# Performance work log

Measured on AMD Instinct MI355X. Metric: run time of the kernel, lower is better.

## Reference

```python
import jax, jax.numpy as jnp
import numpy as np

N = 100000
E = 1600000
IN_C, HID_C, OUT_C = 512, 128, 64
BN_EPS = 1e-5


def _add_self_loops(edge_index, n):
    loops = jnp.arange(n, dtype=edge_index.dtype)
    row = jnp.concatenate([edge_index[0], loops])
    col = jnp.concatenate([edge_index[1], loops])
    return row, col


def gcn_conv(x, W, b, row, col, n):
    # PyG GCNConv: linear first, then symmetric-normalized aggregation
    h = x @ W                                        # [N, out]
    ones = jnp.ones(row.shape[0], dtype=x.dtype)
    deg = jax.ops.segment_sum(ones, col, num_segments=n)   # in-degree incl. self-loop
    dinv = jax.lax.rsqrt(deg)                        # deg >= 1 due to self-loops
    norm = dinv[row] * dinv[col]                     # [E2]
    msg = h[row] * norm[:, None]                     # gather + scale
    out = jax.ops.segment_sum(msg, col, num_segments=n)    # scatter-add
    return out + b


def batchnorm_train(x, gamma, beta):
    mu = jnp.mean(x, axis=0)
    var = jnp.mean((x - mu) ** 2, axis=0)            # biased var, as torch BN
    return (x - mu) * jax.lax.rsqrt(var + BN_EPS) * gamma + beta


def setup_inputs() -> dict:
    key = jax.random.key(0)
    ks = jax.random.split(key, 8)
    x = jax.random.normal(ks[0], (N, IN_C), dtype=jnp.float32)
    edge_index = jax.random.randint(ks[1], (2, E), 0, N, dtype=jnp.int64)
    W1 = jax.random.normal(ks[2], (IN_C, HID_C), dtype=jnp.float32) / np.sqrt(IN_C)
    b1 = jnp.zeros((HID_C,), dtype=jnp.float32)
    gamma = jnp.ones((HID_C,), dtype=jnp.float32)
    beta = jnp.zeros((HID_C,), dtype=jnp.float32)
    W2 = jax.random.normal(ks[3], (HID_C, OUT_C), dtype=jnp.float32) / np.sqrt(HID_C)
    b2 = jnp.zeros((OUT_C,), dtype=jnp.float32)
    return {"x": x, "edge_index": edge_index, "W1": W1, "b1": b1,
            "gamma": gamma, "beta": beta, "W2": W2, "b2": b2}


def reference(x, edge_index, W1, b1, gamma, beta, W2, b2):
    row, col = _add_self_loops(edge_index, N)
    h = gcn_conv(x, W1, b1, row, col, N)
    h = batchnorm_train(h, gamma, beta)
    h = jax.nn.relu(h)
    # dropout: identity (deterministic reference)
    out = gcn_conv(h, W2, b2, row, col, N)
    return out
```

## Files before the change

### kernel.cpp

```cpp
#include <hip/hip_runtime.h>

#define NN 100000
#define NE 1600000
#define INC 512
#define HID 128
#define OUTC 64
#define BN_EPS 1e-5f

#define GS_B 1024
#define NSCB 98

#define NBLK 256
#define CHUNK (NE / NBLK)
#define BSH 8
#define NBUK ((NN + 255) >> 8)

typedef __attribute__((ext_vector_type(8))) short short8v;
typedef __attribute__((ext_vector_type(4))) float f32x4;

__device__ __forceinline__ unsigned short f2bf(float f) {
    unsigned u = __float_as_uint(f);
    u += 0x7FFFu + ((u >> 16) & 1u);
    return (unsigned short)(u >> 16);
}

__device__ __forceinline__ unsigned cvtpk(float lo, float hi) {
    unsigned r;
    asm("v_cvt_pk_bf16_f32 %0, %1, %2" : "=v"(r) : "v"(lo), "v"(hi));
    return r;
}

__device__ __forceinline__ float bflo(unsigned u) { return __uint_as_float(u << 16); }
__device__ __forceinline__ float bfhi(unsigned u) { return __uint_as_float(u & 0xFFFF0000u); }


__global__ __launch_bounds__(256) void k_bhist(const int* __restrict__ col, int* __restrict__ bhist,
                                               float* bnsum, float* bnsumsq) {
    __shared__ int lc[NBUK];
    int tid = threadIdx.x, blk = blockIdx.x;
    if (blk == 0 && tid < HID) { bnsum[tid] = 0.f; bnsumsq[tid] = 0.f; }
    for (int i = tid; i < NBUK; i += 256) lc[i] = 0;
    __syncthreads();
    int s = blk * CHUNK, e = s + CHUNK;
    for (int j = s + tid; j < e; j += 256)
        atomicAdd(&lc[col[j] >> BSH], 1);
    __syncthreads();
    for (int i = tid; i < NBUK; i += 256)
        bhist[i * NBLK + blk] = lc[i];
}

__global__ void k_gscanA(const int* __restrict__ src, int* __restrict__ dst,
                         int* __restrict__ bsum, int n) {
    __shared__ int s[GS_B];
    int tid = threadIdx.x;
    int i = blockIdx.x * GS_B + tid;
    int v = (i < n) ? src[i] : 0;
    s[tid] = v;
    __syncthreads();
    for (int off = 1; off < GS_B; off <<= 1) {
        int t = (tid >= off) ? s[tid - off] : 0;
        __syncthreads();
        s[tid] += t;
        __syncthreads();
    }
    if (i < n) dst[i] = s[tid] - v;
    if (tid == GS_B - 1) bsum[blockIdx.x] = s[tid];
}

__global__ void k_gscanB(int* bsum, int nb) {
    __shared__ int s[256];
    int tid = threadIdx.x;
    for (int i = tid; i < nb; i += blockDim.x) s[i] = bsum[i];
    __syncthreads();
    if (tid == 0) {
        int run = 0;
        for (int i = 0; i < nb; ++i) { int t = s[i]; s[i] = run; run += t; }
    }
    __syncthreads();
    for (int i = tid; i < nb; i += blockDim.x) bsum[i] = s[i];
}

__global__ __launch_bounds__(256) void k_bpart(const int* __restrict__ row, const int* __restrict__ col,
                                               const int* __restrict__ sb, const int* __restrict__ sbsum,
                                               unsigned* __restrict__ ebuk) {
    __shared__ int lcur[NBUK];
    int tid = threadIdx.x, blk = blockIdx.x;
    for (int i = tid; i < NBUK; i += 256) {
        int idx = i * NBLK + blk;
        lcur[i] = sb[idx] + sbsum[idx >> 10];
    }
    __syncthreads();
    int s = blk * CHUNK, e = s + CHUNK;
    for (int j = s + tid; j < e; j += 256) {
        int r = row[j], c = col[j];
        int p = atomicAdd(&lcur[c >> BSH], 1);
        ebuk[p] = (unsigned)r | ((unsigned)(c & 255) << 24);
    }
}

__global__ __launch_bounds__(256) void k_nprep(const unsigned* __restrict__ ebuk,
                                               const int* __restrict__ sb, const int* __restrict__ sbsum,
                                               int* __restrict__ deg, int* __restrict__ rowptr) {
    __shared__ int lc[256];
    __shared__ int sc[256];
    int b = blockIdx.x, tid = threadIdx.x;
    lc[tid] = 0;
    __syncthreads();
    int i0 = b * NBLK;
    int s = sb[i0] + sbsum[i0 >> 10];
    int e2 = (b + 1 < NBUK) ? (sb[i0 + NBLK] + sbsum[(i0 + NBLK) >> 10]) : NE;
    for (int j = s + tid; j < e2; j += 256)
        atomicAdd(&lc[ebuk[j] >> 24], 1);
    __syncthreads();
    int v = lc[tid];
    sc[tid] = v;
    __syncthreads();
    for (int off = 1; off < 256; off <<= 1) {
        int t = (tid >= off) ? sc[tid - off] : 0;
        __syncthreads();
        sc[tid] += t;
        __syncthreads();
    }
    int node = (b << BSH) + tid;
    if (node < NN) {
        deg[node] = v;
        rowptr[node] = s + sc[tid] - v;
    }
    if (b == NBUK - 1 && tid == 0) rowptr[NN] = NE;
}

__global__ __launch_bounds__(256) void k_bfill(const unsigned* __restrict__ ebuk,
                                               const int* __restrict__ sb, const int* __restrict__ sbsum,
                                               const int* __restrict__ rowptr, const int* __restrict__ deg,
                                               unsigned* __restrict__ csr) {
    __shared__ int lcur[256];
    int b = blockIdx.x, tid = threadIdx.x;
    int node0 = b << BSH;
    int node = node0 + tid;
    lcur[tid] = (node < NN) ? rowptr[node] : 0;
    __syncthreads();
    int i0 = b * NBLK;
    int s = sb[i0] + sbsum[i0 >> 10];
    int e2 = (b + 1 < NBUK) ? (sb[i0 + NBLK] + sbsum[(i0 + NBLK) >> 10]) : NE;
    for (int j = s + tid; j < e2; j += 256) {
        unsigned rc = ebuk[j];
        int li = rc >> 24;
        int r = rc & 0xFFFFFF;
        int p = atomicAdd(&lcur[li], 1);
        csr[p] = (unsigned)r | ((unsigned)deg[r] << 17);
    }
}


__global__ void k_prepW1(const float* __restrict__ W1, unsigned short* __restrict__ W1T) {
    int i = blockIdx.x * 256 + threadIdx.x;
    int k = i >> 7, n = i & 127;
    W1T[(size_t)n * INC + k] = f2bf(W1[i]);
}


#define G1BK 64
#define APAD 72

__global__ __launch_bounds__(256) void k_gemm1m(const float* __restrict__ x,
                                                const unsigned short* __restrict__ W1T,
                                                unsigned short* __restrict__ h1b) {
    __shared__ unsigned short As[64][APAD];
    __shared__ unsigned short Bs[128][APAD];
    int tid = threadIdx.x;
    int m0 = blockIdx.x * 64;
    int w = tid >> 6;
    int lane = tid & 63;

    f32x4 acc[4][2];
    #pragma unroll
    for (int mr = 0; mr < 4; ++mr)
        #pragma unroll
        for (int cb = 0; cb < 2; ++cb) acc[mr][cb] = (f32x4){0.f, 0.f, 0.f, 0.f};

    int ar = tid >> 2;
    int ak = (tid & 3) * 16;
    int arow = m0 + ar; if (arow >= NN) arow = NN - 1;
    const float* xr = x + (size_t)arow * INC;
    int br = tid >> 1;
    int bk = (tid & 1) * 32;
    const unsigned short* wr = W1T + (size_t)br * INC;

    int frow = lane & 15;
    int fk = (lane >> 4) * 8;

    float4 pv[4];
    short8v pb[4];
    #pragma unroll
    for (int q = 0; q < 4; ++q) pv[q] = *(const float4*)(xr + ak + q * 4);
    #pragma unroll
    for (int q = 0; q < 4; ++q) pb[q] = *(const short8v*)(wr + bk + q * 8);

    for (int k0 = 0; k0 < INC; k0 += G1BK) {
        #pragma unroll
        for (int q = 0; q < 4; ++q)
            *(uint2*)&As[ar][ak + q * 4] = make_uint2(cvtpk(pv[q].x, pv[q].y), cvtpk(pv[q].z, pv[q].w));
        #pragma unroll
        for (int q = 0; q < 4; ++q)
            *(short8v*)&Bs[br][bk + q * 8] = pb[q];
        __syncthreads();
        if (k0 + G1BK < INC) {
            #pragma unroll
            for (int q = 0; q < 4; ++q) pv[q] = *(const float4*)(xr + k0 + G1BK + ak + q * 4);
            #pragma unroll
            for (int q = 0; q < 4; ++q) pb[q] = *(const short8v*)(wr + k0 + G1BK + bk + q * 8);
        }
        #pragma unroll
        for (int kk = 0; kk < G1BK; kk += 32) {
            short8v a[4], b[2];
            #pragma unroll
            for (int mr = 0; mr < 4; ++mr)
                a[mr] = *(const short8v*)&As[16 * mr + frow][kk + fk];
            #pragma unroll
            for (int cb = 0; cb < 2; ++cb)
                b[cb] = *(const short8v*)&Bs[32 * w + 16 * cb + frow][kk + fk];
            #pragma unroll
            for (int mr = 0; mr < 4; ++mr)
                #pragma unroll
                for (int cb = 0; cb < 2; ++cb)
                    acc[mr][cb] = __builtin_amdgcn_mfma_f32_16x16x32_bf16(b[cb], a[mr], acc[mr][cb], 0, 0, 0);
        }
        __syncthreads();
    }
    int ncol = lane & 15;
    int r4 = (lane >> 4) * 4;
    #pragma unroll
    for (int mr = 0; mr < 4; ++mr) {
        int node = m0 + 16 * mr + ncol;
        if (node < NN) {
            #pragma unroll
            for (int cb = 0; cb < 2; ++cb) {
                int ch = 32 * w + 16 * cb + r4;
                *(uint2*)&h1b[(size_t)node * HID + ch] =
                    make_uint2(cvtpk(acc[mr][cb][0], acc[mr][cb][1]),
                               cvtpk(acc[mr][cb][2], acc[mr][cb][3]));
            }
        }
    }
}


__global__ __launch_bounds__(256) void k_agg1(const unsigned short* __restrict__ h1b,
                                              const int* __restrict__ deg,
                                              const int* __restrict__ rowptr, const unsigned* __restrict__ csr,
                                              const float* __restrict__ b1, unsigned* __restrict__ aggb) {
    int node = blockIdx.x * 4 + (threadIdx.x >> 6);
    int lane = threadIdx.x & 63;
    const unsigned* hp = (const unsigned*)h1b;
    size_t base = (size_t)node * 64 + lane;
    float dnf = (float)(deg[node] + 1);
    float di = rsqrtf(dnf);
    float wself = di * di;
    unsigned hv = hp[base];
    float sx = wself * bflo(hv);
    float sy = wself * bfhi(hv);
    int s = rowptr[node], e = rowptr[node + 1];
    int j = s;
    for (; j + 4 <= e; j += 4) {
        unsigned c0 = csr[j], c1 = csr[j + 1], c2 = csr[j + 2], c3 = csr[j + 3];
        int r0 = c0 & 0x1FFFF, r1 = c1 & 0x1FFFF, r2 = c2 & 0x1FFFF, r3 = c3 & 0x1FFFF;
        unsigned v0 = hp[(size_t)r0 * 64 + lane];
        unsigned v1 = hp[(size_t)r1 * 64 + lane];
        unsigned v2 = hp[(size_t)r2 * 64 + lane];
        unsigned v3 = hp[(size_t)r3 * 64 + lane];
        float w0 = rsqrtf(dnf * (float)((c0 >> 17) + 1));
        float w1 = rsqrtf(dnf * (float)((c1 >> 17) + 1));
        float w2 = rsqrtf(dnf * (float)((c2 >> 17) + 1));
        float w3 = rsqrtf(dnf * (float)((c3 >> 17) + 1));
        sx = fmaf(w0, bflo(v0), sx); sy = fmaf(w0, bfhi(v0), sy);
        sx = fmaf(w1, bflo(v1), sx); sy = fmaf(w1, bfhi(v1), sy);
        sx = fmaf(w2, bflo(v2), sx); sy = fmaf(w2, bfhi(v2), sy);
        sx = fmaf(w3, bflo(v3), sx); sy = fmaf(w3, bfhi(v3), sy);
    }
    for (; j < e; ++j) {
        unsigned c = csr[j];
        int r = c & 0x1FFFF;
        unsigned v = hp[(size_t)r * 64 + lane];
        float ww = rsqrtf(dnf * (float)((c >> 17) + 1));
        sx = fmaf(ww, bflo(v), sx); sy = fmaf(ww, bfhi(v), sy);
    }
    float2 bb = ((const float2*)b1)[lane];
    aggb[base] = cvtpk(sx + bb.x, sy + bb.y);
}


__global__ __launch_bounds__(256) void k_bnstats(const unsigned* __restrict__ aggb,
                                                 float* __restrict__ bnsum, float* __restrict__ bnsumsq) {
    __shared__ float4 ss[256], sq[256];
    int g = threadIdx.x & 31;
    int h = threadIdx.x >> 5;
    float4 fs = make_float4(0.f, 0.f, 0.f, 0.f);
    float4 fq = make_float4(0.f, 0.f, 0.f, 0.f);
    int rows_per_block = (NN + gridDim.x - 1) / gridDim.x;
    int r0 = blockIdx.x * rows_per_block;
    int r1 = r0 + rows_per_block; if (r1 > NN) r1 = NN;
    for (int r = r0 + h; r < r1; r += 8) {
        uint2 u = *(const uint2*)(aggb + (size_t)r * 64 + 2 * g);
        float a0 = bflo(u.x), a1 = bfhi(u.x), a2 = bflo(u.y), a3 = bfhi(u.y);
        fs.x += a0; fs.y += a1; fs.z += a2; fs.w += a3;
        fq.x += a0 * a0; fq.y += a1 * a1; fq.z += a2 * a2; fq.w += a3 * a3;
    }
    ss[threadIdx.x] = fs; sq[threadIdx.x] = fq;
    __syncthreads();
    if (threadIdx.x < 32) {
        float4 as = ss[threadIdx.x], aq = sq[threadIdx.x];
        #pragma unroll
        for (int k = 1; k < 8; ++k) {
            float4 bs = ss[k * 32 + threadIdx.x], bq = sq[k * 32 + threadIdx.x];
            as.x += bs.x; as.y += bs.y; as.z += bs.z; as.w += bs.w;
            aq.x += bq.x; aq.y += bq.y; aq.z += bq.z; aq.w += bq.w;
        }
        atomicAdd(&bnsum[4 * g + 0], as.x); atomicAdd(&bnsum[4 * g + 1], as.y);
        atomicAdd(&bnsum[4 * g + 2], as.z); atomicAdd(&bnsum[4 * g + 3], as.w);
        atomicAdd(&bnsumsq[4 * g + 0], aq.x); atomicAdd(&bnsumsq[4 * g + 1], aq.y);
        atomicAdd(&bnsumsq[4 * g + 2], aq.z); atomicAdd(&bnsumsq[4 * g + 3], aq.w);
    }
}

__global__ void k_bnfinal(const float* __restrict__ bnsum, const float* __restrict__ bnsumsq,
                          const float* __restrict__ gamma, const float* __restrict__ beta,
                          float* __restrict__ bnscale, float* __restrict__ bnshift) {
    int c = threadIdx.x;
    if (c < HID) {
        float mu = bnsum[c] / (float)NN;
        float var = bnsumsq[c] / (float)NN - mu * mu;
        float sc = gamma[c] * rsqrtf(var + BN_EPS);
        bnscale[c] = sc;
        bnshift[c] = beta[c] - mu * sc;
    }
}


__global__ __launch_bounds__(256) void k_gemm2(const unsigned* __restrict__ aggb, const float* __restrict__ W2,
                                               const float* __restrict__ bnscale, const float* __restrict__ bnshift,
                                               unsigned short* __restrict__ h2b) {
    __shared__ float As2[32][66];
    __shared__ float Bs2[32][OUTC];
    int tid = threadIdx.x;
    int m0 = blockIdx.x * 64;
    int tx = tid & 15, ty = tid >> 4;
    float acc[4][4];
    #pragma unroll
    for (int r = 0; r < 4; ++r)
        #pragma unroll
        for (int c = 0; c < 4; ++c) acc[r][c] = 0.f;

    int am = tid >> 3;
    int ak = (tid & 7) * 4;
    int bk = tid >> 4;
    int bc = (tid & 15) * 4;

    for (int k0 = 0; k0 < HID; k0 += 32) {
        #pragma unroll
        for (int h = 0; h < 2; ++h) {
            int m = am + h * 32;
            int rowi = m0 + m; if (rowi >= NN) rowi = NN - 1;
            uint2 u = *(const uint2*)(aggb + (size_t)rowi * 64 + ((k0 + ak) >> 1));
            float4 sc = *(const float4*)(bnscale + k0 + ak);
            float4 sh = *(const float4*)(bnshift + k0 + ak);
            As2[ak + 0][m] = fmaxf(fmaf(bflo(u.x), sc.x, sh.x), 0.f);
            As2[ak + 1][m] = fmaxf(fmaf(bfhi(u.x), sc.y, sh.y), 0.f);
            As2[ak + 2][m] = fmaxf(fmaf(bflo(u.y), sc.z, sh.z), 0.f);
            As2[ak + 3][m] = fmaxf(fmaf(bfhi(u.y), sc.w, sh.w), 0.f);
        }
        #pragma unroll
        for (int h = 0; h < 2; ++h) {
            int k = bk + h * 16;
            *(float4*)&Bs2[k][bc] = *(const float4*)(W2 + (size_t)(k0 + k) * OUTC + bc);
        }
        __syncthreads();
        #pragma unroll
        for (int k = 0; k < 32; ++k) {
            float a[4];
            #pragma unroll
            for (int r = 0; r < 4; ++r) a[r] = As2[k][ty * 4 + r];
            float4 b = *(const float4*)&Bs2[k][tx * 4];
            #pragma unroll
            for (int r = 0; r < 4; ++r) {
                acc[r][0] = fmaf(a[r], b.x, acc[r][0]);
                acc[r][1] = fmaf(a[r], b.y, acc[r][1]);
                acc[r][2] = fmaf(a[r], b.z, acc[r][2]);
                acc[r][3] = fmaf(a[r], b.w, acc[r][3]);
            }
        }
        __syncthreads();
    }
    #pragma unroll
    for (int r = 0; r < 4; ++r) {
        int m = m0 + ty * 4 + r;
        if (m < NN) {
            *(uint2*)(h2b + (size_t)m * OUTC + tx * 4) =
                make_uint2(cvtpk(acc[r][0], acc[r][1]), cvtpk(acc[r][2], acc[r][3]));
        }
    }
}


__global__ __launch_bounds__(256) void k_agg2(const unsigned short* __restrict__ h2b,
                                              const int* __restrict__ deg,
                                              const int* __restrict__ rowptr, const unsigned* __restrict__ csr,
                                              const float* __restrict__ b2, float* __restrict__ out) {
    int node = blockIdx.x * 4 + (threadIdx.x >> 6);
    int lane = threadIdx.x & 63;
    int l32 = lane & 31;
    const unsigned* hp = (const unsigned*)h2b;
    float dnf = (float)(deg[node] + 1);
    float di = rsqrtf(dnf);
    float wself = di * di;
    float sx = 0.f, sy = 0.f;
    if (lane < 32) {
        unsigned u = hp[(size_t)node * 32 + l32];
        sx = wself * bflo(u);
        sy = wself * bfhi(u);
    }
    int s = rowptr[node], e = rowptr[node + 1];
    int j = s + (lane >> 5);
    for (; j + 2 < e; j += 4) {
        unsigned c0 = csr[j], c1 = csr[j + 2];
        int r0 = c0 & 0x1FFFF, r1 = c1 & 0x1FFFF;
        unsigned v0 = hp[(size_t)r0 * 32 + l32];
        unsigned v1 = hp[(size_t)r1 * 32 + l32];
        float w0 = rsqrtf(dnf * (float)((c0 >> 17) + 1));
        float w1 = rsqrtf(dnf * (float)((c1 >> 17) + 1));
        sx = fmaf(w0, bflo(v0), sx); sy = fmaf(w0, bfhi(v0), sy);
        sx = fmaf(w1, bflo(v1), sx); sy = fmaf(w1, bfhi(v1), sy);
    }
    if (j < e) {
        unsigned c = csr[j];
        int r = c & 0x1FFFF;
        unsigned v = hp[(size_t)r * 32 + l32];
        float ww = rsqrtf(dnf * (float)((c >> 17) + 1));
        sx = fmaf(ww, bflo(v), sx); sy = fmaf(ww, bfhi(v), sy);
    }
    sx += __shfl_xor(sx, 32);
    sy += __shfl_xor(sy, 32);
    if (lane < 32) {
        float2 bb = ((const float2*)b2)[l32];
        ((float2*)out)[(size_t)node * 32 + l32] = make_float2(sx + bb.x, sy + bb.y);
    }
}


extern "C" void kernel_launch(void* const* d_in, const int* in_sizes, int n_in,
                              void* d_out, int out_size, void* d_ws, size_t ws_size,
                              hipStream_t stream) {
    const float* x     = (const float*)d_in[0];
    const int*   ei    = (const int*)d_in[1];
    const float* W1    = (const float*)d_in[2];
    const float* b1    = (const float*)d_in[3];
    const float* gamma = (const float*)d_in[4];
    const float* beta  = (const float*)d_in[5];
    const float* W2    = (const float*)d_in[6];
    const float* b2    = (const float*)d_in[7];
    const int* row = ei;
    const int* col = ei + NE;
    float* out = (float*)d_out;

    char* wp = (char*)d_ws;
    auto alloc = [&](size_t bytes) -> void* {
        void* p = (void*)wp;
        wp += (bytes + 255) & ~(size_t)255;
        return p;
    };
    unsigned short* h1b = (unsigned short*)alloc((size_t)NN * HID * 2);
    unsigned* aggb = (unsigned*)alloc((size_t)NN * HID * 2);
    unsigned short* h2b = (unsigned short*)alloc((size_t)NN * OUTC * 2);
    int*   deg     = (int*)alloc((size_t)NN * 4);
    float* bnsum   = (float*)alloc(HID * 4);
    float* bnsumsq = (float*)alloc(HID * 4);
    float* bnscale = (float*)alloc(HID * 4);
    float* bnshift = (float*)alloc(HID * 4);
    int*   rowptr  = (int*)alloc((size_t)(NN + 1) * 4);
    int*   bhist   = (int*)alloc((size_t)NBUK * NBLK * 4);
    int*   bsum2   = (int*)alloc(NSCB * 4);
    unsigned* ebuk = (unsigned*)alloc((size_t)NE * 4);
    unsigned* csr  = (unsigned*)alloc((size_t)NE * 4);
    unsigned short* W1T = (unsigned short*)alloc((size_t)HID * INC * 2);

    hipLaunchKernelGGL(k_bhist,  dim3(NBLK), dim3(256), 0, stream, col, bhist, bnsum, bnsumsq);
    hipLaunchKernelGGL(k_gscanA, dim3(NSCB), dim3(GS_B), 0, stream, bhist, bhist, bsum2, NBUK * NBLK);
    hipLaunchKernelGGL(k_gscanB, dim3(1), dim3(128), 0, stream, bsum2, NSCB);
    hipLaunchKernelGGL(k_bpart,  dim3(NBLK), dim3(256), 0, stream, row, col, bhist, bsum2, ebuk);
    hipLaunchKernelGGL(k_nprep,  dim3(NBUK), dim3(256), 0, stream, ebuk, bhist, bsum2, deg, rowptr);
    hipLaunchKernelGGL(k_bfill,  dim3(NBUK), dim3(256), 0, stream, ebuk, bhist, bsum2, rowptr, deg, csr);
    hipLaunchKernelGGL(k_prepW1, dim3(256), dim3(256), 0, stream, W1, W1T);
    hipLaunchKernelGGL(k_gemm1m, dim3((NN + 63) / 64), dim3(256), 0, stream, x, W1T, h1b);
    hipLaunchKernelGGL(k_agg1,   dim3(NN / 4), dim3(256), 0, stream, h1b, deg, rowptr, csr, b1, aggb);
    hipLaunchKernelGGL(k_bnstats, dim3(256), dim3(256), 0, stream, aggb, bnsum, bnsumsq);
    hipLaunchKernelGGL(k_bnfinal, dim3(1), dim3(128), 0, stream, bnsum, bnsumsq, gamma, beta, bnscale, bnshift);
    hipLaunchKernelGGL(k_gemm2,  dim3((NN + 63) / 64), dim3(256), 0, stream, aggb, W2, bnscale, bnshift, h2b);
    hipLaunchKernelGGL(k_agg2,   dim3(NN / 4), dim3(256), 0, stream, h2b, deg, rowptr, csr, b2, out);
}
```

Baseline: 325.6 us.

## Fold small helper kernels into neighbors and deepen gather unroll in aggregations

Removes three tiny launches. The W1 transpose moves into the histogram kernel, the block-sum scan is recomputed redundantly in shared memory by each consumer kernel, and the BN finalize is computed at the start of each gemm2 block. The aggregation loops get an 8-wide unroll so more independent gathers are in flight per wavefront. This trades launch overhead and serial gaps for a little redundant per-block work and extra register pressure.

```diff
diff --git a/kernel.cpp b/kernel.cpp
--- a/kernel.cpp
+++ b/kernel.cpp
@@ -33,20 +33,35 @@
 __device__ __forceinline__ float bflo(unsigned u) { return __uint_as_float(u << 16); }
 __device__ __forceinline__ float bfhi(unsigned u) { return __uint_as_float(u & 0xFFFF0000u); }
 
-
-__global__ __launch_bounds__(256) void k_bhist(const int* __restrict__ col, int* __restrict__ bhist,
-                                               float* bnsum, float* bnsumsq) {
+__device__ __forceinline__ void scan_bsum(const int* __restrict__ bsum2, int* spref) {
+    int tid = threadIdx.x;
+    if (tid < NSCB) spref[tid] = bsum2[tid];
+    __syncthreads();
+    if (tid == 0) {
+        int run = 0;
+        #pragma unroll 1
+        for (int i = 0; i < NSCB; ++i) { int t = spref[i]; spref[i] = run; run += t; }
+    }
+    __syncthreads();
+}
+
+
+__global__ __launch_bounds__(256) void k_pre(const int* __restrict__ col, int* __restrict__ bhist,
+                                             const float* __restrict__ W1, unsigned short* __restrict__ W1T,
+                                             float* bnsum, float* bnsumsq) {
     __shared__ int lc[NBUK];
     int tid = threadIdx.x, blk = blockIdx.x;
+    int i = blk * 256 + tid;
+    W1T[(size_t)(i & 127) * INC + (i >> 7)] = f2bf(W1[i]);
     if (blk == 0 && tid < HID) { bnsum[tid] = 0.f; bnsumsq[tid] = 0.f; }
-    for (int i = tid; i < NBUK; i += 256) lc[i] = 0;
+    for (int q = tid; q < NBUK; q += 256) lc[q] = 0;
     __syncthreads();
     int s = blk * CHUNK, e = s + CHUNK;
     for (int j = s + tid; j < e; j += 256)
         atomicAdd(&lc[col[j] >> BSH], 1);
     __syncthreads();
-    for (int i = tid; i < NBUK; i += 256)
-        bhist[i * NBLK + blk] = lc[i];
+    for (int q = tid; q < NBUK; q += 256)
+        bhist[q * NBLK + blk] = lc[q];
 }
 
 __global__ void k_gscanA(const int* __restrict__ src, int* __restrict__ dst,
@@ -67,27 +82,16 @@
     if (tid == GS_B - 1) bsum[blockIdx.x] = s[tid];
 }
 
-__global__ void k_gscanB(int* bsum, int nb) {
-    __shared__ int s[256];
-    int tid = threadIdx.x;
-    for (int i = tid; i < nb; i += blockDim.x) s[i] = bsum[i];
-    __syncthreads();
-    if (tid == 0) {
-        int run = 0;
-        for (int i = 0; i < nb; ++i) { int t = s[i]; s[i] = run; run += t; }
-    }
-    __syncthreads();
-    for (int i = tid; i < nb; i += blockDim.x) bsum[i] = s[i];
-}
-
 __global__ __launch_bounds__(256) void k_bpart(const int* __restrict__ row, const int* __restrict__ col,
-                                               const int* __restrict__ sb, const int* __restrict__ sbsum,
+                                               const int* __restrict__ sb, const int* __restrict__ bsum2,
                                                unsigned* __restrict__ ebuk) {
     __shared__ int lcur[NBUK];
+    __shared__ int spref[NSCB];
     int tid = threadIdx.x, blk = blockIdx.x;
+    scan_bsum(bsum2, spref);
     for (int i = tid; i < NBUK; i += 256) {
         int idx = i * NBLK + blk;
-        lcur[i] = sb[idx] + sbsum[idx >> 10];
+        lcur[i] = sb[idx] + spref[idx >> 10];
     }
     __syncthreads();
     int s = blk * CHUNK, e = s + CHUNK;
@@ -99,16 +103,18 @@
 }
 
 __global__ __launch_bounds__(256) void k_nprep(const unsigned* __restrict__ ebuk,
-                                               const int* __restrict__ sb, const int* __restrict__ sbsum,
+                                               const int* __restrict__ sb, const int* __restrict__ bsum2,
                                                int* __restrict__ deg, int* __restrict__ rowptr) {
     __shared__ int lc[256];
     __shared__ int sc[256];
+    __shared__ int spref[NSCB];
     int b = blockIdx.x, tid = threadIdx.x;
+    scan_bsum(bsum2, spref);
     lc[tid] = 0;
     __syncthreads();
     int i0 = b * NBLK;
-    int s = sb[i0] + sbsum[i0 >> 10];
-    int e2 = (b + 1 < NBUK) ? (sb[i0 + NBLK] + sbsum[(i0 + NBLK) >> 10]) : NE;
+    int s = sb[i0] + spref[i0 >> 10];
+    int e2 = (b + 1 < NBUK) ? (sb[i0 + NBLK] + spref[(i0 + NBLK) >> 10]) : NE;
     for (int j = s + tid; j < e2; j += 256)
         atomicAdd(&lc[ebuk[j] >> 24], 1);
     __syncthreads();
@@ -130,18 +136,20 @@
 }
 
 __global__ __launch_bounds__(256) void k_bfill(const unsigned* __restrict__ ebuk,
-                                               const int* __restrict__ sb, const int* __restrict__ sbsum,
+                                               const int* __restrict__ sb, const int* __restrict__ bsum2,
                                                const int* __restrict__ rowptr, const int* __restrict__ deg,
                                                unsigned* __restrict__ csr) {
     __shared__ int lcur[256];
+    __shared__ int spref[NSCB];
     int b = blockIdx.x, tid = threadIdx.x;
+    scan_bsum(bsum2, spref);
     int node0 = b << BSH;
     int node = node0 + tid;
     lcur[tid] = (node < NN) ? rowptr[node] : 0;
     __syncthreads();
     int i0 = b * NBLK;
-    int s = sb[i0] + sbsum[i0 >> 10];
-    int e2 = (b + 1 < NBUK) ? (sb[i0 + NBLK] + sbsum[(i0 + NBLK) >> 10]) : NE;
+    int s = sb[i0] + spref[i0 >> 10];
+    int e2 = (b + 1 < NBUK) ? (sb[i0 + NBLK] + spref[(i0 + NBLK) >> 10]) : NE;
     for (int j = s + tid; j < e2; j += 256) {
         unsigned rc = ebuk[j];
         int li = rc >> 24;
@@ -149,13 +157,6 @@
         int p = atomicAdd(&lcur[li], 1);
         csr[p] = (unsigned)r | ((unsigned)deg[r] << 17);
     }
-}
-
-
-__global__ void k_prepW1(const float* __restrict__ W1, unsigned short* __restrict__ W1T) {
-    int i = blockIdx.x * 256 + threadIdx.x;
-    int k = i >> 7, n = i & 127;
-    W1T[(size_t)n * INC + k] = f2bf(W1[i]);
 }
 
 
@@ -261,13 +262,40 @@
     float sy = wself * bfhi(hv);
     int s = rowptr[node], e = rowptr[node + 1];
     int j = s;
+    for (; j + 8 <= e; j += 8) {
+        unsigned c0 = csr[j],     c1 = csr[j + 1], c2 = csr[j + 2], c3 = csr[j + 3];
+        unsigned c4 = csr[j + 4], c5 = csr[j + 5], c6 = csr[j + 6], c7 = csr[j + 7];
+        unsigned v0 = hp[(size_t)(c0 & 0x1FFFF) * 64 + lane];
+        unsigned v1 = hp[(size_t)(c1 & 0x1FFFF) * 64 + lane];
+        unsigned v2 = hp[(size_t)(c2 & 0x1FFFF) * 64 + lane];
+        unsigned v3 = hp[(size_t)(c3 & 0x1FFFF) * 64 + lane];
+        unsigned v4 = hp[(size_t)(c4 & 0x1FFFF) * 64 + lane];
+        unsigned v5 = hp[(size_t)(c5 & 0x1FFFF) * 64 + lane];
+        unsigned v6 = hp[(size_t)(c6 & 0x1FFFF) * 64 + lane];
+        unsigned v7 = hp[(size_t)(c7 & 0x1FFFF) * 64 + lane];
+        float w0 = rsqrtf(dnf * (float)((c0 >> 17) + 1));
+        float w1 = rsqrtf(dnf * (float)((c1 >> 17) + 1));
+        float w2 = rsqrtf(dnf * (float)((c2 >> 17) + 1));
+        float w3 = rsqrtf(dnf * (float)((c3 >> 17) + 1));
+        float w4 = rsqrtf(dnf * (float)((c4 >> 17) + 1));
+        float w5 = rsqrtf(dnf * (float)((c5 >> 17) + 1));
+        float w6 = rsqrtf(dnf * (float)((c6 >> 17) + 1));
+        float w7 = rsqrtf(dnf * (float)((c7 >> 17) + 1));
+        sx = fmaf(w0, bflo(v0), sx); sy = fmaf(w0, bfhi(v0), sy);
+        sx = fmaf(w1, bflo(v1), sx); sy = fmaf(w1, bfhi(v1), sy);
+        sx = fmaf(w2, bflo(v2), sx); sy = fmaf(w2, bfhi(v2), sy);
+        sx = fmaf(w3, bflo(v3), sx); sy = fmaf(w3, bfhi(v3), sy);
+        sx = fmaf(w4, bflo(v4), sx); sy = fmaf(w4, bfhi(v4), sy);
+        sx = fmaf(w5, bflo(v5), sx); sy = fmaf(w5, bfhi(v5), sy);
+        sx = fmaf(w6, bflo(v6), sx); sy = fmaf(w6, bfhi(v6), sy);
+        sx = fmaf(w7, bflo(v7), sx); sy = fmaf(w7, bfhi(v7), sy);
+    }
     for (; j + 4 <= e; j += 4) {
         unsigned c0 = csr[j], c1 = csr[j + 1], c2 = csr[j + 2], c3 = csr[j + 3];
-        int r0 = c0 & 0x1FFFF, r1 = c1 & 0x1FFFF, r2 = c2 & 0x1FFFF, r3 = c3 & 0x1FFFF;
-        unsigned v0 = hp[(size_t)r0 * 64 + lane];
-        unsigned v1 = hp[(size_t)r1 * 64 + lane];
-        unsigned v2 = hp[(size_t)r2 * 64 + lane];
-        unsigned v3 = hp[(size_t)r3 * 64 + lane];
+        unsigned v0 = hp[(size_t)(c0 & 0x1FFFF) * 64 + lane];
+        unsigned v1 = hp[(size_t)(c1 & 0x1FFFF) * 64 + lane];
+        unsigned v2 = hp[(size_t)(c2 & 0x1FFFF) * 64 + lane];
+        unsigned v3 = hp[(size_t)(c3 & 0x1FFFF) * 64 + lane];
         float w0 = rsqrtf(dnf * (float)((c0 >> 17) + 1));
         float w1 = rsqrtf(dnf * (float)((c1 >> 17) + 1));
         float w2 = rsqrtf(dnf * (float)((c2 >> 17) + 1));
@@ -279,8 +307,7 @@
     }
     for (; j < e; ++j) {
         unsigned c = csr[j];
-        int r = c & 0x1FFFF;
-        unsigned v = hp[(size_t)r * 64 + lane];
+        unsigned v = hp[(size_t)(c & 0x1FFFF) * 64 + lane];
         float ww = rsqrtf(dnf * (float)((c >> 17) + 1));
         sx = fmaf(ww, bflo(v), sx); sy = fmaf(ww, bfhi(v), sy);
     }
@@ -322,26 +349,23 @@
     }
 }
 
-__global__ void k_bnfinal(const float* __restrict__ bnsum, const float* __restrict__ bnsumsq,
-                          const float* __restrict__ gamma, const float* __restrict__ beta,
-                          float* __restrict__ bnscale, float* __restrict__ bnshift) {
-    int c = threadIdx.x;
-    if (c < HID) {
-        float mu = bnsum[c] / (float)NN;
-        float var = bnsumsq[c] / (float)NN - mu * mu;
-        float sc = gamma[c] * rsqrtf(var + BN_EPS);
-        bnscale[c] = sc;
-        bnshift[c] = beta[c] - mu * sc;
-    }
-}
-
 
 __global__ __launch_bounds__(256) void k_gemm2(const unsigned* __restrict__ aggb, const float* __restrict__ W2,
-                                               const float* __restrict__ bnscale, const float* __restrict__ bnshift,
+                                               const float* __restrict__ bnsum, const float* __restrict__ bnsumsq,
+                                               const float* __restrict__ gamma, const float* __restrict__ beta,
                                                unsigned short* __restrict__ h2b) {
     __shared__ float As2[32][66];
     __shared__ float Bs2[32][OUTC];
+    __shared__ float bnsc[HID], bnsh[HID];
     int tid = threadIdx.x;
+    if (tid < HID) {
+        float mu = bnsum[tid] / (float)NN;
+        float var = bnsumsq[tid] / (float)NN - mu * mu;
+        float sc = gamma[tid] * rsqrtf(var + BN_EPS);
+        bnsc[tid] = sc;
+        bnsh[tid] = beta[tid] - mu * sc;
+    }
+    __syncthreads();
     int m0 = blockIdx.x * 64;
     int tx = tid & 15, ty = tid >> 4;
     float acc[4][4];
@@ -361,8 +385,8 @@
             int m = am + h * 32;
             int rowi = m0 + m; if (rowi >= NN) rowi = NN - 1;
             uint2 u = *(const uint2*)(aggb + (size_t)rowi * 64 + ((k0 + ak) >> 1));
-            float4 sc = *(const float4*)(bnscale + k0 + ak);
-            float4 sh = *(const float4*)(bnshift + k0 + ak);
+            float4 sc = *(const float4*)&bnsc[k0 + ak];
+            float4 sh = *(const float4*)&bnsh[k0 + ak];
             As2[ak + 0][m] = fmaxf(fmaf(bflo(u.x), sc.x, sh.x), 0.f);
             As2[ak + 1][m] = fmaxf(fmaf(bfhi(u.x), sc.y, sh.y), 0.f);
             As2[ak + 2][m] = fmaxf(fmaf(bflo(u.y), sc.z, sh.z), 0.f);
@@ -420,11 +444,25 @@
     }
     int s = rowptr[node], e = rowptr[node + 1];
     int j = s + (lane >> 5);
+    for (; j + 6 < e; j += 8) {
+        unsigned c0 = csr[j], c1 = csr[j + 2], c2 = csr[j + 4], c3 = csr[j + 6];
+        unsigned v0 = hp[(size_t)(c0 & 0x1FFFF) * 32 + l32];
+        unsigned v1 = hp[(size_t)(c1 & 0x1FFFF) * 32 + l32];
+        unsigned v2 = hp[(size_t)(c2 & 0x1FFFF) * 32 + l32];
+        unsigned v3 = hp[(size_t)(c3 & 0x1FFFF) * 32 + l32];
+        float w0 = rsqrtf(dnf * (float)((c0 >> 17) + 1));
+        float w1 = rsqrtf(dnf * (float)((c1 >> 17) + 1));
+        float w2 = rsqrtf(dnf * (float)((c2 >> 17) + 1));
+        float w3 = rsqrtf(dnf * (float)((c3 >> 17) + 1));
+        sx = fmaf(w0, bflo(v0), sx); sy = fmaf(w0, bfhi(v0), sy);
+        sx = fmaf(w1, bflo(v1), sx); sy = fmaf(w1, bfhi(v1), sy);
+        sx = fmaf(w2, bflo(v2), sx); sy = fmaf(w2, bfhi(v2), sy);
+        sx = fmaf(w3, bflo(v3), sx); sy = fmaf(w3, bfhi(v3), sy);
+    }
     for (; j + 2 < e; j += 4) {
         unsigned c0 = csr[j], c1 = csr[j + 2];
-        int r0 = c0 & 0x1FFFF, r1 = c1 & 0x1FFFF;
-        unsigned v0 = hp[(size_t)r0 * 32 + l32];
-        unsigned v1 = hp[(size_t)r1 * 32 + l32];
+        unsigned v0 = hp[(size_t)(c0 & 0x1FFFF) * 32 + l32];
+        unsigned v1 = hp[(size_t)(c1 & 0x1FFFF) * 32 + l32];
         float w0 = rsqrtf(dnf * (float)((c0 >> 17) + 1));
         float w1 = rsqrtf(dnf * (float)((c1 >> 17) + 1));
         sx = fmaf(w0, bflo(v0), sx); sy = fmaf(w0, bfhi(v0), sy);
@@ -432,8 +470,7 @@
     }
     if (j < e) {
         unsigned c = csr[j];
-        int r = c & 0x1FFFF;
-        unsigned v = hp[(size_t)r * 32 + l32];
+        unsigned v = hp[(size_t)(c & 0x1FFFF) * 32 + l32];
         float ww = rsqrtf(dnf * (float)((c >> 17) + 1));
         sx = fmaf(ww, bflo(v), sx); sy = fmaf(ww, bfhi(v), sy);
     }
@@ -473,8 +510,6 @@
     int*   deg     = (int*)alloc((size_t)NN * 4);
     float* bnsum   = (float*)alloc(HID * 4);
     float* bnsumsq = (float*)alloc(HID * 4);
-    float* bnscale = (float*)alloc(HID * 4);
-    float* bnshift = (float*)alloc(HID * 4);
     int*   rowptr  = (int*)alloc((size_t)(NN + 1) * 4);
     int*   bhist   = (int*)alloc((size_t)NBUK * NBLK * 4);
     int*   bsum2   = (int*)alloc(NSCB * 4);
@@ -482,17 +517,14 @@
     unsigned* csr  = (unsigned*)alloc((size_t)NE * 4);
     unsigned short* W1T = (unsigned short*)alloc((size_t)HID * INC * 2);
 
-    hipLaunchKernelGGL(k_bhist,  dim3(NBLK), dim3(256), 0, stream, col, bhist, bnsum, bnsumsq);
+    hipLaunchKernelGGL(k_pre,    dim3(NBLK), dim3(256), 0, stream, col, bhist, W1, W1T, bnsum, bnsumsq);
     hipLaunchKernelGGL(k_gscanA, dim3(NSCB), dim3(GS_B), 0, stream, bhist, bhist, bsum2, NBUK * NBLK);
-    hipLaunchKernelGGL(k_gscanB, dim3(1), dim3(128), 0, stream, bsum2, NSCB);
     hipLaunchKernelGGL(k_bpart,  dim3(NBLK), dim3(256), 0, stream, row, col, bhist, bsum2, ebuk);
     hipLaunchKernelGGL(k_nprep,  dim3(NBUK), dim3(256), 0, stream, ebuk, bhist, bsum2, deg, rowptr);
     hipLaunchKernelGGL(k_bfill,  dim3(NBUK), dim3(256), 0, stream, ebuk, bhist, bsum2, rowptr, deg, csr);
-    hipLaunchKernelGGL(k_prepW1, dim3(256), dim3(256), 0, stream, W1, W1T);
     hipLaunchKernelGGL(k_gemm1m, dim3((NN + 63) / 64), dim3(256), 0, stream, x, W1T, h1b);
     hipLaunchKernelGGL(k_agg1,   dim3(NN / 4), dim3(256), 0, stream, h1b, deg, rowptr, csr, b1, aggb);
     hipLaunchKernelGGL(k_bnstats, dim3(256), dim3(256), 0, stream, aggb, bnsum, bnsumsq);
-    hipLaunchKernelGGL(k_bnfinal, dim3(1), dim3(128), 0, stream, bnsum, bnsumsq, gamma, beta, bnscale, bnshift);
-    hipLaunchKernelGGL(k_gemm2,  dim3((NN + 63) / 64), dim3(256), 0, stream, aggb, W2, bnscale, bnshift, h2b);
+    hipLaunchKernelGGL(k_gemm2,  dim3((NN + 63) / 64), dim3(256), 0, stream, aggb, W2, bnsum, bnsumsq, gamma, beta, h2b);
     hipLaunchKernelGGL(k_agg2,   dim3(NN / 4), dim3(256), 0, stream, h2b, deg, rowptr, csr, b2, out);
 }
```

Measured after the change: 313.0 us. 1.04x faster.
